# Kernel tuning notes

Measured on AMD Instinct MI355X. Metric: run time of the kernel, lower is better.

The kernel has to match this reference:

```python
import jax, jax.numpy as jnp
import numpy as np

B, T, C = 8, 2048, 1024
DFF = 4 * C
EPS = 1e-5


def _ln(h, w, b):
    mu = jnp.mean(h, axis=-1, keepdims=True)
    var = jnp.mean((h - mu) ** 2, axis=-1, keepdims=True)
    return (h - mu) * jax.lax.rsqrt(var + EPS) * w + b


def setup_inputs() -> dict:
    key = jax.random.key(0)
    ks = jax.random.split(key, 8)
    s = lambda fan_in: 1.0 / np.sqrt(fan_in)
    return {
        "x": jax.random.normal(ks[0], (B, T, C), jnp.float32),
        "w_router": jax.random.normal(ks[1], (1, C), jnp.float32) * s(C),
        "ln1_w": jnp.ones((C,), jnp.float32),
        "ln1_b": jnp.zeros((C,), jnp.float32),
        "w_qkv": jax.random.normal(ks[2], (3 * C, C), jnp.float32) * s(C),
        "b_qkv": jnp.zeros((3 * C,), jnp.float32),
        "w_o": jax.random.normal(ks[3], (C, C), jnp.float32) * s(C),
        "b_o": jnp.zeros((C,), jnp.float32),
        "ln2_w": jnp.ones((C,), jnp.float32),
        "ln2_b": jnp.zeros((C,), jnp.float32),
        "w_fc": jax.random.normal(ks[4], (DFF, C), jnp.float32) * s(C),
        "b_fc": jnp.zeros((DFF,), jnp.float32),
        "w_proj": jax.random.normal(ks[5], (C, DFF), jnp.float32) * s(DFF),
        "b_proj": jnp.zeros((C,), jnp.float32),
        "top_k": 1024,
        "n_head": 16,
    }


def _gpt2_block(h, ln1_w, ln1_b, w_qkv, b_qkv, w_o, b_o, ln2_w, ln2_b,
                w_fc, b_fc, w_proj, b_proj, n_head):
    Bq, S, Cm = h.shape
    dh = Cm // n_head
    a = _ln(h, ln1_w, ln1_b)
    qkv = a @ w_qkv.T + b_qkv                         # [B,S,3C]
    q, k, v = jnp.split(qkv, 3, axis=-1)
    q = q.reshape(Bq, S, n_head, dh)
    k = k.reshape(Bq, S, n_head, dh)
    v = v.reshape(Bq, S, n_head, dh)
    scores = jnp.einsum("bqhd,bkhd->bhqk", q, k) / np.sqrt(dh)
    causal = jnp.tril(jnp.ones((S, S), bool))
    scores = jnp.where(causal, scores, jnp.finfo(scores.dtype).min)
    probs = jax.nn.softmax(scores, axis=-1)
    attn = jnp.einsum("bhqk,bkhd->bqhd", probs, v).reshape(Bq, S, Cm)
    h = h + attn @ w_o.T + b_o
    m = _ln(h, ln2_w, ln2_b)
    mlp = jax.nn.gelu(m @ w_fc.T + b_fc, approximate=False) @ w_proj.T + b_proj
    return h + mlp


def reference(x, w_router, ln1_w, ln1_b, w_qkv, b_qkv, w_o, b_o,
              ln2_w, ln2_b, w_fc, b_fc, w_proj, b_proj, top_k, n_head):
    # STEP 1: router logits + top-k tokens (sorted by position)
    logits = (x @ w_router.T)[..., 0]                  # [B,T]
    weights, idx = jax.lax.top_k(logits, top_k)        # [B,K]
    order = jnp.argsort(idx, axis=1)
    idx = jnp.take_along_axis(idx, order, axis=1)
    weights = jnp.take_along_axis(weights, order, axis=1)
    # STEP 2: gather reduced sequence and run the block
    tokens = jnp.take_along_axis(x, idx[..., None], axis=1)   # [B,K,C]
    processed = _gpt2_block(tokens, ln1_w, ln1_b, w_qkv, b_qkv, w_o, b_o,
                            ln2_w, ln2_b, w_fc, b_fc, w_proj, b_proj, n_head)
    # STEP 3: weighted scatter-add combine
    src = processed * weights[..., None]
    out = jax.vmap(lambda xb, ib, sb: xb.at[ib].add(sb))(x, idx, src)
    return out
```

## Files before the change

kernel.cpp:

```cpp
#include <hip/hip_runtime.h>
#include <hip/hip_bf16.h>

#define B_ 8
#define T_ 2048
#define C_ 1024
#define S_ 1024
#define H_ 16
#define DH_ 64
#define DFF_ 4096
#define M_ (B_*S_)

typedef __attribute__((ext_vector_type(8))) short bf16x8;
typedef __attribute__((ext_vector_type(4))) float f32x4;

__device__ __forceinline__ short f2bf(float f) {
  __hip_bfloat16 h = __float2bfloat16(f);
  return *reinterpret_cast<short*>(&h);
}
__device__ __forceinline__ float bf2f(short s) {
  __hip_bfloat16 h = *reinterpret_cast<__hip_bfloat16*>(&s);
  return __bfloat162float(h);
}

typedef const __attribute__((address_space(1))) unsigned int* gas_p;
typedef __attribute__((address_space(3))) unsigned int* las_p;
__device__ __forceinline__ void gload_lds16(const void* g, void* l) {
  __builtin_amdgcn_global_load_lds((gas_p)g, (las_p)l, 16, 0, 0);
}

__global__ __launch_bounds__(256) void k_router(const float* __restrict__ x,
    const float* __restrict__ wr, float* __restrict__ logits) {
  int tok = blockIdx.x * 4 + (threadIdx.x >> 6);
  int l = threadIdx.x & 63;
  const float* xr = x + (size_t)tok * C_;
  float s = 0.f;
  #pragma unroll
  for (int j = 0; j < C_/64; ++j) s += xr[l + 64*j] * wr[l + 64*j];
  #pragma unroll
  for (int m = 32; m; m >>= 1) s += __shfl_xor(s, m);
  if (l == 0) logits[tok] = s;
}

__global__ __launch_bounds__(1024) void k_topk(const float* __restrict__ logits,
    int* __restrict__ idx, float* __restrict__ wts) {
  __shared__ unsigned long long key[2048];
  int b = blockIdx.x, t = threadIdx.x;
  for (int i = t; i < T_; i += 1024) {
    float v = logits[(size_t)b*T_ + i];
    unsigned u = __float_as_uint(v);
    unsigned so = u ^ ((u >> 31) ? 0xFFFFFFFFu : 0x80000000u);
    key[i] = ((unsigned long long)(~so) << 32) | (unsigned)i;
  }
  __syncthreads();
  for (int k = 2; k <= 2048; k <<= 1) {
    for (int j = k >> 1; j > 0; j >>= 1) {
      int i = ((t & ~(j-1)) << 1) | (t & (j-1));
      int ix = i | j;
      unsigned long long a = key[i], c = key[ix];
      bool up = ((i & k) == 0);
      if ((a > c) == up) { key[i] = c; key[ix] = a; }
      __syncthreads();
    }
  }
  unsigned long long a = key[t];
  __syncthreads();
  unsigned i0 = (unsigned)(a & 0xFFFFFFFFu);
  unsigned so = ~(unsigned)(a >> 32);
  unsigned bits = (so & 0x80000000u) ? (so ^ 0x80000000u) : ~so;
  key[t] = ((unsigned long long)i0 << 32) | bits;
  __syncthreads();
  for (int k = 2; k <= 1024; k <<= 1) {
    for (int j = k >> 1; j > 0; j >>= 1) {
      if (t < 512) {
        int i = ((t & ~(j-1)) << 1) | (t & (j-1));
        int ix = i | j;
        unsigned long long a2 = key[i], c2 = key[ix];
        bool up = ((i & k) == 0);
        if ((a2 > c2) == up) { key[i] = c2; key[ix] = a2; }
      }
      __syncthreads();
    }
  }
  idx[(size_t)b*S_ + t] = (int)(key[t] >> 32);
  wts[(size_t)b*S_ + t] = __uint_as_float((unsigned)(key[t] & 0xFFFFFFFFu));
}

__global__ __launch_bounds__(256) void k_cvt(const float* __restrict__ s,
    short* __restrict__ d, int n4) {
  int i = blockIdx.x * 256 + threadIdx.x;
  if (i >= n4) return;
  float4 v = ((const float4*)s)[i];
  short4 o;
  o.x = f2bf(v.x); o.y = f2bf(v.y); o.z = f2bf(v.z); o.w = f2bf(v.w);
  ((short4*)d)[i] = o;
}

template<bool GATHER>
__global__ __launch_bounds__(256) void k_ln(const float* __restrict__ x,
    const int* __restrict__ idx, float* __restrict__ hbuf,
    short* __restrict__ obf, const float* __restrict__ g,
    const float* __restrict__ beta) {
  __shared__ float red[8];
  int row = blockIdx.x;
  const float* src;
  if (GATHER) {
    int b = row >> 10, k = row & 1023;
    src = x + ((size_t)b*T_ + idx[b*S_ + k]) * C_;
  } else {
    src = hbuf + (size_t)row * C_;
  }
  int t = threadIdx.x;
  float4 v = *(const float4*)(src + t*4);
  float s  = v.x + v.y + v.z + v.w;
  float s2 = v.x*v.x + v.y*v.y + v.z*v.z + v.w*v.w;
  #pragma unroll
  for (int m = 32; m; m >>= 1) { s += __shfl_xor(s, m); s2 += __shfl_xor(s2, m); }
  int w = t >> 6, lane = t & 63;
  if (lane == 0) { red[w] = s; red[w+4] = s2; }
  __syncthreads();
  s  = red[0]+red[1]+red[2]+red[3];
  s2 = red[4]+red[5]+red[6]+red[7];
  float mu = s * (1.f/(float)C_);
  float var = s2 * (1.f/(float)C_) - mu*mu;
  float rs = rsqrtf(var + 1e-5f);
  int c0 = t*4;
  float4 gw = *(const float4*)(g + c0);
  float4 bw = *(const float4*)(beta + c0);
  short4 o;
  o.x = f2bf((v.x-mu)*rs*gw.x + bw.x);
  o.y = f2bf((v.y-mu)*rs*gw.y + bw.y);
  o.z = f2bf((v.z-mu)*rs*gw.z + bw.z);
  o.w = f2bf((v.w-mu)*rs*gw.w + bw.w);
  *(short4*)(obf + (size_t)row*C_ + c0) = o;
  if (GATHER) *(float4*)(hbuf + (size_t)row*C_ + c0) = v;
}

#define EPI_BF16 0
#define EPI_GELU 1
#define EPI_ADD32 2

__device__ __forceinline__ float gelu_fast(float v) {
  float z = 0.7978845608f * (v + 0.044715f * v * v * v);
  float e = __expf(2.f * z);
  return v - v * __builtin_amdgcn_rcpf(e + 1.f);
}

template<int BM, int BN, int EPI>
__global__ __launch_bounds__(256) void k_gemm4(
    const short* __restrict__ A, int lda,
    const short* __restrict__ Bp, int ldb,
    void* __restrict__ Cp, int ldc,
    const float* __restrict__ bias,
    int nNt, int Ktot) {
  constexpr int ACH = BM*64/8/256;
  constexpr int BCH = BN*64/8/256;
  __shared__ short As[BM*64];
  __shared__ short Bs[BN*64];
  int nwg = gridDim.x, orig = blockIdx.x;
  int q8 = nwg >> 3, r8 = nwg & 7;
  int xcd = orig & 7, loc = orig >> 3;
  int wg = (xcd < r8 ? xcd*(q8+1) : r8*(q8+1) + (xcd-r8)*q8) + loc;
  int bm = wg / nNt, bn = wg % nNt;
  const short* Ar = A + (size_t)bm*BM*lda;
  const short* Br = Bp + (size_t)bn*BN*ldb;
  constexpr int WM = BM/2, WN = BN/2, FM = WM/16, FN = WN/16;
  int t = threadIdx.x, lane = t & 63, w = t >> 6;
  int wm = w >> 1, wn = w & 1;
  int lr = lane & 15, kq = lane >> 4;
  f32x4 acc[FM][FN] = {};
  for (int k0 = 0; k0 < Ktot; k0 += 64) {
    #pragma unroll
    for (int c = 0; c < ACH; ++c) {
      int ch = c*256 + t;
      int row = ch >> 3, sq = (ch & 7) ^ (row & 7);
      gload_lds16(Ar + (size_t)row*lda + (k0 + sq*8), &As[ch*8]);
    }
    #pragma unroll
    for (int c = 0; c < BCH; ++c) {
      int ch = c*256 + t;
      int row = ch >> 3, sq = (ch & 7) ^ (row & 7);
      gload_lds16(Br + (size_t)row*ldb + (k0 + sq*8), &Bs[ch*8]);
    }
    asm volatile("s_waitcnt vmcnt(0)" ::: "memory");
    __syncthreads();
    bf16x8 af[2][FM], bfv[2][FN];
    #pragma unroll
    for (int ks = 0; ks < 2; ++ks) {
      #pragma unroll
      for (int i = 0; i < FM; ++i) {
        int ra = wm*WM + i*16 + lr;
        af[ks][i] = *(const bf16x8*)&As[ra*64 + ((((ks<<2)+kq) ^ (ra & 7)) << 3)];
      }
      #pragma unroll
      for (int j = 0; j < FN; ++j) {
        int rb = wn*WN + j*16 + lr;
        bfv[ks][j] = *(const bf16x8*)&Bs[rb*64 + ((((ks<<2)+kq) ^ (rb & 7)) << 3)];
      }
    }
    #pragma unroll
    for (int ks = 0; ks < 2; ++ks)
      #pragma unroll
      for (int i = 0; i < FM; ++i)
        #pragma unroll
        for (int j = 0; j < FN; ++j)
          acc[i][j] = __builtin_amdgcn_mfma_f32_16x16x32_bf16(bfv[ks][j], af[ks][i], acc[i][j], 0, 0, 0);
    __syncthreads();
  }
  int mrow0 = bm*BM + wm*WM + lr;
  int ncol0 = bn*BN + wn*WN + (kq << 2);
  #pragma unroll
  for (int i = 0; i < FM; ++i) {
    int row = mrow0 + i*16;
    #pragma unroll
    for (int j = 0; j < FN; ++j) {
      int col = ncol0 + j*16;
      float4 bv = bias ? *(const float4*)(bias + col) : make_float4(0.f,0.f,0.f,0.f);
      float v0 = acc[i][j][0] + bv.x, v1 = acc[i][j][1] + bv.y;
      float v2 = acc[i][j][2] + bv.z, v3 = acc[i][j][3] + bv.w;
      if (EPI == EPI_ADD32) {
        float* Co = (float*)Cp + (size_t)row*ldc + col;
        float4 old = *(float4*)Co;
        old.x += v0; old.y += v1; old.z += v2; old.w += v3;
        *(float4*)Co = old;
      } else {
        if (EPI == EPI_GELU) {
          v0 = gelu_fast(v0); v1 = gelu_fast(v1);
          v2 = gelu_fast(v2); v3 = gelu_fast(v3);
        }
        short4 o; o.x = f2bf(v0); o.y = f2bf(v1); o.z = f2bf(v2); o.w = f2bf(v3);
        *(short4*)((short*)Cp + (size_t)row*ldc + col) = o;
      }
    }
  }
}

__global__ __launch_bounds__(256) void k_vt(const short* __restrict__ qkv,
                                            short* __restrict__ vt) {
  __shared__ short tile[64][65];
  int blk = blockIdx.x;
  int s0 = (blk & 15) << 6;
  int bh = blk >> 4;
  int b = bh >> 4, h = bh & 15;
  const short* src = qkv + (size_t)b*S_*3*C_ + 2*C_ + h*DH_;
  int t = threadIdx.x;
  #pragma unroll
  for (int it = 0; it < 16; ++it) {
    int e = it*256 + t;
    int r = e >> 6, d = e & 63;
    tile[d][r] = src[(size_t)(s0 + r)*3*C_ + d];
  }
  __syncthreads();
  short* dst = vt + (size_t)bh*DH_*S_ + s0;
  #pragma unroll
  for (int it = 0; it < 16; ++it) {
    int e = it*256 + t;
    int d2 = e >> 6, c = e & 63;
    dst[(size_t)d2*S_ + c] = tile[d2][c];
  }
}

__global__ __launch_bounds__(256) void k_fattn(
    const short* __restrict__ qkv, const short* __restrict__ vt,
    short* __restrict__ attnb) {
  __shared__ short Ks[128*64];
  __shared__ short Vs[64*128];
  __shared__ short Ps[4][32*136];
  int qt = blockIdx.x;
  int bh = blockIdx.y;
  int b = bh >> 4, h = bh & 15;
  int t = threadIdx.x, lane = t & 63, w = t >> 6;
  int lr = lane & 15, kq = lane >> 4;
  const short* Qbase = qkv + ((size_t)b*S_ + qt*128)*3*C_ + h*DH_;
  const short* Kbase = qkv + (size_t)b*S_*3*C_ + C_ + h*DH_;
  const short* Vtb   = vt + (size_t)bh*DH_*S_;

  #pragma unroll
  for (int c = 0; c < 4; ++c) {
    int ch = c*256 + t;
    int row = ch >> 3, sq = (ch & 7) ^ (row & 7);
    gload_lds16(Qbase + (size_t)row*3*C_ + sq*8, &Ks[ch*8]);
  }
  asm volatile("s_waitcnt vmcnt(0)" ::: "memory");
  __syncthreads();
  bf16x8 qf[2][2];
  #pragma unroll
  for (int ks = 0; ks < 2; ++ks)
    #pragma unroll
    for (int i = 0; i < 2; ++i) {
      int rq = w*32 + i*16 + lr;
      qf[ks][i] = *(const bf16x8*)&Ks[rq*64 + ((((ks<<2)+kq) ^ (rq & 7)) << 3)];
    }
  __syncthreads();

  f32x4 o[2][4] = {};
  float m_i[2] = {-3.0e38f, -3.0e38f};
  float l_i[2] = {0.f, 0.f};
  short* Pw = &Ps[w][0];

  for (int j128 = 0; j128 <= qt; ++j128) {
    #pragma unroll
    for (int c = 0; c < 4; ++c) {
      int ch = c*256 + t;
      int row = ch >> 3, sq = (ch & 7) ^ (row & 7);
      gload_lds16(Kbase + (size_t)(j128*128 + row)*3*C_ + sq*8, &Ks[ch*8]);
    }
    #pragma unroll
    for (int c = 0; c < 4; ++c) {
      int ch = c*256 + t;
      int row = ch >> 4, cc = ch & 15, sq = cc ^ ((row & 7) << 1);
      gload_lds16(Vtb + (size_t)row*S_ + (j128*128 + sq*8), &Vs[ch*8]);
    }
    asm volatile("s_waitcnt vmcnt(0)" ::: "memory");
    __syncthreads();

    f32x4 s[2][8] = {};
    #pragma unroll
    for (int ks = 0; ks < 2; ++ks) {
      bf16x8 kf[8];
      #pragma unroll
      for (int j = 0; j < 8; ++j) {
        int rk = j*16 + lr;
        kf[j] = *(const bf16x8*)&Ks[rk*64 + ((((ks<<2)+kq) ^ (rk & 7)) << 3)];
      }
      #pragma unroll
      for (int i = 0; i < 2; ++i)
        #pragma unroll
        for (int j = 0; j < 8; ++j)
          s[i][j] = __builtin_amdgcn_mfma_f32_16x16x32_bf16(kf[j], qf[ks][i], s[i][j], 0, 0, 0);
    }

    bool diag = (j128 == qt);
    #pragma unroll
    for (int i = 0; i < 2; ++i) {
      int qrow = w*32 + i*16 + lr;
      float rmax = -3.0e38f;
      #pragma unroll
      for (int j = 0; j < 8; ++j)
        #pragma unroll
        for (int r = 0; r < 4; ++r) {
          int col = j*16 + (kq<<2) + r;
          float v = s[i][j][r] * 0.125f;
          if (diag && col > qrow) v = -3.0e38f;
          s[i][j][r] = v;
          rmax = fmaxf(rmax, v);
        }
      rmax = fmaxf(rmax, __shfl_xor(rmax, 16));
      rmax = fmaxf(rmax, __shfl_xor(rmax, 32));
      float mnew = fmaxf(m_i[i], rmax);
      float alpha = __expf(m_i[i] - mnew);
      m_i[i] = mnew;
      float rsum = 0.f;
      #pragma unroll
      for (int j = 0; j < 8; ++j)
        #pragma unroll
        for (int r = 0; r < 4; ++r) {
          float p = __expf(s[i][j][r] - mnew);
          s[i][j][r] = p;
          rsum += p;
        }
      rsum += __shfl_xor(rsum, 16);
      rsum += __shfl_xor(rsum, 32);
      l_i[i] = l_i[i]*alpha + rsum;
      #pragma unroll
      for (int jo = 0; jo < 4; ++jo)
        #pragma unroll
        for (int r = 0; r < 4; ++r)
          o[i][jo][r] *= alpha;
    }

    #pragma unroll
    for (int i = 0; i < 2; ++i)
      #pragma unroll
      for (int j = 0; j < 8; ++j) {
        short4 pk;
        pk.x = f2bf(s[i][j][0]); pk.y = f2bf(s[i][j][1]);
        pk.z = f2bf(s[i][j][2]); pk.w = f2bf(s[i][j][3]);
        int prow = i*16 + lr;
        *(short4*)&Pw[prow*136 + j*16 + (kq<<2)] = pk;
      }
    __syncthreads();

    #pragma unroll
    for (int sstep = 0; sstep < 4; ++sstep) {
      bf16x8 pf[2], vf[4];
      #pragma unroll
      for (int i = 0; i < 2; ++i) {
        int prow = i*16 + lr;
        pf[i] = *(const bf16x8*)&Pw[prow*136 + sstep*32 + (kq<<3)];
      }
      #pragma unroll
      for (int jo = 0; jo < 4; ++jo) {
        int rv = jo*16 + lr;
        int cc = (sstep*4 + kq) ^ ((rv & 7) << 1);
        vf[jo] = *(const bf16x8*)&Vs[rv*128 + cc*8];
      }
      #pragma unroll
      for (int i = 0; i < 2; ++i)
        #pragma unroll
        for (int jo = 0; jo < 4; ++jo)
          o[i][jo] = __builtin_amdgcn_mfma_f32_16x16x32_bf16(vf[jo], pf[i], o[i][jo], 0, 0, 0);
    }
    __syncthreads();
  }

  #pragma unroll
  for (int i = 0; i < 2; ++i) {
    float inv = 1.f / l_i[i];
    int q = qt*128 + w*32 + i*16 + lr;
    #pragma unroll
    for (int jo = 0; jo < 4; ++jo) {
      int d = jo*16 + (kq<<2);
      short4 ov;
      ov.x = f2bf(o[i][jo][0]*inv); ov.y = f2bf(o[i][jo][1]*inv);
      ov.z = f2bf(o[i][jo][2]*inv); ov.w = f2bf(o[i][jo][3]*inv);
      *(short4*)&attnb[((size_t)b*S_ + q)*C_ + h*DH_ + d] = ov;
    }
  }
}

__global__ void k_copy(const float* __restrict__ src, float* __restrict__ dst,
                       size_t n4) {
  size_t i = (size_t)blockIdx.x*256 + threadIdx.x;
  size_t stride = (size_t)gridDim.x*256;
  for (; i < n4; i += stride) ((float4*)dst)[i] = ((const float4*)src)[i];
}

__global__ __launch_bounds__(256) void k_scatter(const float* __restrict__ x,
    const int* __restrict__ idx, const float* __restrict__ wts,
    const float* __restrict__ hbuf, float* __restrict__ out) {
  int row = blockIdx.x;
  int b = row >> 10, k = row & 1023;
  int tk = idx[(size_t)b*S_ + k];
  float wv = wts[(size_t)b*S_ + k];
  size_t o  = ((size_t)b*T_ + tk)*C_ + threadIdx.x*4;
  size_t hs = (size_t)row*C_ + threadIdx.x*4;
  float4 xv = *(const float4*)(x + o);
  float4 hv = *(const float4*)(hbuf + hs);
  xv.x += wv*hv.x; xv.y += wv*hv.y; xv.z += wv*hv.z; xv.w += wv*hv.w;
  *(float4*)(out + o) = xv;
}

extern "C" void kernel_launch(void* const* d_in, const int* in_sizes, int n_in,
                              void* d_out, int out_size, void* d_ws, size_t ws_size,
                              hipStream_t stream) {
  const float* x     = (const float*)d_in[0];
  const float* wrt   = (const float*)d_in[1];
  const float* ln1w  = (const float*)d_in[2];
  const float* ln1b  = (const float*)d_in[3];
  const float* wqkv  = (const float*)d_in[4];
  const float* bqkv  = (const float*)d_in[5];
  const float* wo    = (const float*)d_in[6];
  const float* bo    = (const float*)d_in[7];
  const float* ln2w  = (const float*)d_in[8];
  const float* ln2b  = (const float*)d_in[9];
  const float* wfc   = (const float*)d_in[10];
  const float* bfc   = (const float*)d_in[11];
  const float* wproj = (const float*)d_in[12];
  const float* bproj = (const float*)d_in[13];
  float* out = (float*)d_out;

  char* p = (char*)d_ws;
  auto alloc = [&](size_t bytes) {
    char* r = p; p += (bytes + 255) & ~(size_t)255; return r;
  };
  float* logits = (float*)alloc((size_t)B_*T_*4);
  int*   idx    = (int*)  alloc((size_t)B_*S_*4);
  float* wts    = (float*)alloc((size_t)B_*S_*4);
  float* hbuf   = (float*)alloc((size_t)M_*C_*4);
  short* abuf   = (short*)alloc((size_t)M_*C_*2);
  short* qkvb   = (short*)alloc((size_t)M_*3*C_*2);
  short* vtb    = (short*)alloc((size_t)B_*H_*DH_*S_*2);
  short* attnb  = (short*)alloc((size_t)M_*C_*2);
  short* fcb    = (short*)alloc((size_t)M_*DFF_*2);
  short* wqkvb  = (short*)alloc((size_t)3*C_*C_*2);
  short* wob    = (short*)alloc((size_t)C_*C_*2);
  short* wfcb   = (short*)alloc((size_t)DFF_*C_*2);
  short* wprojb = (short*)alloc((size_t)C_*DFF_*2);
  if (ws_size < (size_t)(p - (char*)d_ws)) return;

  k_cvt<<<dim3(3*C_*C_/4/256), dim3(256), 0, stream>>>(wqkv, wqkvb, 3*C_*C_/4);
  k_cvt<<<dim3(C_*C_/4/256),   dim3(256), 0, stream>>>(wo, wob, C_*C_/4);
  k_cvt<<<dim3(DFF_*C_/4/256), dim3(256), 0, stream>>>(wfc, wfcb, DFF_*C_/4);
  k_cvt<<<dim3(C_*DFF_/4/256), dim3(256), 0, stream>>>(wproj, wprojb, C_*DFF_/4);

  k_router<<<dim3(B_*T_/4), dim3(256), 0, stream>>>(x, wrt, logits);
  k_topk<<<dim3(B_), dim3(1024), 0, stream>>>(logits, idx, wts);

  k_ln<true><<<dim3(M_), dim3(256), 0, stream>>>(x, idx, hbuf, abuf, ln1w, ln1b);

  k_gemm4<128,128,EPI_BF16>
    <<<dim3((M_/128)*(3*C_/128)), dim3(256), 0, stream>>>(
      abuf, C_, wqkvb, C_, qkvb, 3*C_, bqkv, 3*C_/128, C_);

  k_vt<<<dim3(B_*H_*(S_/64)), dim3(256), 0, stream>>>(qkvb, vtb);

  k_fattn<<<dim3(S_/128, B_*H_), dim3(256), 0, stream>>>(qkvb, vtb, attnb);

  k_gemm4<128,128,EPI_ADD32>
    <<<dim3((M_/128)*(C_/128)), dim3(256), 0, stream>>>(
      attnb, C_, wob, C_, hbuf, C_, bo, C_/128, C_);

  k_ln<false><<<dim3(M_), dim3(256), 0, stream>>>(nullptr, nullptr, hbuf, abuf, ln2w, ln2b);

  k_gemm4<128,128,EPI_GELU>
    <<<dim3((M_/128)*(DFF_/128)), dim3(256), 0, stream>>>(
      abuf, C_, wfcb, C_, fcb, DFF_, bfc, DFF_/128, C_);

  k_gemm4<128,128,EPI_ADD32>
    <<<dim3((M_/128)*(C_/128)), dim3(256), 0, stream>>>(
      fcb, DFF_, wprojb, DFF_, hbuf, C_, bproj, C_/128, DFF_);

  k_copy<<<dim3(2048), dim3(256), 0, stream>>>(x, out, (size_t)B_*T_*C_/4);
  k_scatter<<<dim3(M_), dim3(256), 0, stream>>>(x, idx, wts, hbuf, out);
}
```

Baseline: 560.5 us.

## Double-buffer 64-wide K tiles in flash attention, read V directly from global

```diff
diff --git a/kernel.cpp b/kernel.cpp
--- a/kernel.cpp
+++ b/kernel.cpp
@@ -259,12 +259,11 @@
   }
 }
 
-__global__ __launch_bounds__(256) void k_fattn(
+__global__ __launch_bounds__(256, 4) void k_fattn(
     const short* __restrict__ qkv, const short* __restrict__ vt,
     short* __restrict__ attnb) {
-  __shared__ short Ks[128*64];
-  __shared__ short Vs[64*128];
-  __shared__ short Ps[4][32*136];
+  __shared__ short Ks[2][64*64];
+  __shared__ short Ps[4][32*72];
   int qt = blockIdx.x;
   int bh = blockIdx.y;
   int b = bh >> 4, h = bh & 15;
@@ -274,73 +273,77 @@
   const short* Kbase = qkv + (size_t)b*S_*3*C_ + C_ + h*DH_;
   const short* Vtb   = vt + (size_t)bh*DH_*S_;
 
+  short* Qs = &Ks[0][0];
   #pragma unroll
   for (int c = 0; c < 4; ++c) {
     int ch = c*256 + t;
     int row = ch >> 3, sq = (ch & 7) ^ (row & 7);
-    gload_lds16(Qbase + (size_t)row*3*C_ + sq*8, &Ks[ch*8]);
+    gload_lds16(Qbase + (size_t)row*3*C_ + sq*8, &Qs[ch*8]);
   }
   asm volatile("s_waitcnt vmcnt(0)" ::: "memory");
-  __syncthreads();
+  __builtin_amdgcn_s_barrier();
   bf16x8 qf[2][2];
   #pragma unroll
   for (int ks = 0; ks < 2; ++ks)
     #pragma unroll
     for (int i = 0; i < 2; ++i) {
       int rq = w*32 + i*16 + lr;
-      qf[ks][i] = *(const bf16x8*)&Ks[rq*64 + ((((ks<<2)+kq) ^ (rq & 7)) << 3)];
-    }
-  __syncthreads();
+      qf[ks][i] = *(const bf16x8*)&Qs[rq*64 + ((((ks<<2)+kq) ^ (rq & 7)) << 3)];
+    }
+  asm volatile("s_waitcnt lgkmcnt(0)" ::: "memory");
+  __builtin_amdgcn_sched_barrier(0);
+  __builtin_amdgcn_s_barrier();
+
+  auto stageK = [&](int buf, int jj) {
+    #pragma unroll
+    for (int c = 0; c < 2; ++c) {
+      int ch = c*256 + t;
+      int row = ch >> 3, sq = (ch & 7) ^ (row & 7);
+      gload_lds16(Kbase + (size_t)(jj*64 + row)*3*C_ + sq*8, &Ks[buf][ch*8]);
+    }
+  };
+  stageK(0, 0);
 
   f32x4 o[2][4] = {};
   float m_i[2] = {-3.0e38f, -3.0e38f};
   float l_i[2] = {0.f, 0.f};
   short* Pw = &Ps[w][0];
-
-  for (int j128 = 0; j128 <= qt; ++j128) {
-    #pragma unroll
-    for (int c = 0; c < 4; ++c) {
-      int ch = c*256 + t;
-      int row = ch >> 3, sq = (ch & 7) ^ (row & 7);
-      gload_lds16(Kbase + (size_t)(j128*128 + row)*3*C_ + sq*8, &Ks[ch*8]);
-    }
-    #pragma unroll
-    for (int c = 0; c < 4; ++c) {
-      int ch = c*256 + t;
-      int row = ch >> 4, cc = ch & 15, sq = cc ^ ((row & 7) << 1);
-      gload_lds16(Vtb + (size_t)row*S_ + (j128*128 + sq*8), &Vs[ch*8]);
-    }
+  int NTl = 2*qt + 2;
+
+  for (int jj = 0; jj < NTl; ++jj) {
+    int cur = jj & 1;
     asm volatile("s_waitcnt vmcnt(0)" ::: "memory");
-    __syncthreads();
-
-    f32x4 s[2][8] = {};
+    __builtin_amdgcn_s_barrier();
+    if (jj + 1 < NTl) stageK(cur ^ 1, jj + 1);
+
+    f32x4 s[2][4] = {};
     #pragma unroll
     for (int ks = 0; ks < 2; ++ks) {
-      bf16x8 kf[8];
-      #pragma unroll
-      for (int j = 0; j < 8; ++j) {
+      bf16x8 kf[4];
+      #pragma unroll
+      for (int j = 0; j < 4; ++j) {
         int rk = j*16 + lr;
-        kf[j] = *(const bf16x8*)&Ks[rk*64 + ((((ks<<2)+kq) ^ (rk & 7)) << 3)];
+        kf[j] = *(const bf16x8*)&Ks[cur][rk*64 + ((((ks<<2)+kq) ^ (rk & 7)) << 3)];
       }
       #pragma unroll
       for (int i = 0; i < 2; ++i)
         #pragma unroll
-        for (int j = 0; j < 8; ++j)
+        for (int j = 0; j < 4; ++j)
           s[i][j] = __builtin_amdgcn_mfma_f32_16x16x32_bf16(kf[j], qf[ks][i], s[i][j], 0, 0, 0);
     }
 
-    bool diag = (j128 == qt);
+    bool maskTile = (jj >= 2*qt);
     #pragma unroll
     for (int i = 0; i < 2; ++i) {
-      int qrow = w*32 + i*16 + lr;
+      int qrow = qt*128 + w*32 + i*16 + lr;
       float rmax = -3.0e38f;
       #pragma unroll
-      for (int j = 0; j < 8; ++j)
+      for (int j = 0; j < 4; ++j)
         #pragma unroll
         for (int r = 0; r < 4; ++r) {
-          int col = j*16 + (kq<<2) + r;
+          int colg = jj*64 + j*16 + (kq<<2) + r;
           float v = s[i][j][r] * 0.125f;
-          if (diag && col > qrow) v = -3.0e38f;
+          if (maskTile && colg > qrow) v = -3.0e38f;
           s[i][j][r] = v;
           rmax = fmaxf(rmax, v);
         }
@@ -351,12 +354,12 @@
       m_i[i] = mnew;
       float rsum = 0.f;
       #pragma unroll
-      for (int j = 0; j < 8; ++j)
+      for (int j = 0; j < 4; ++j)
         #pragma unroll
         for (int r = 0; r < 4; ++r) {
-          float p = __expf(s[i][j][r] - mnew);
-          s[i][j][r] = p;
-          rsum += p;
+          float pv = __expf(s[i][j][r] - mnew);
+          s[i][j][r] = pv;
+          rsum += pv;
         }
       rsum += __shfl_xor(rsum, 16);
       rsum += __shfl_xor(rsum, 32);
@@ -371,36 +374,30 @@
     #pragma unroll
     for (int i = 0; i < 2; ++i)
       #pragma unroll
-      for (int j = 0; j < 8; ++j) {
+      for (int j = 0; j < 4; ++j) {
         short4 pk;
         pk.x = f2bf(s[i][j][0]); pk.y = f2bf(s[i][j][1]);
         pk.z = f2bf(s[i][j][2]); pk.w = f2bf(s[i][j][3]);
-        int prow = i*16 + lr;
-        *(short4*)&Pw[prow*136 + j*16 + (kq<<2)] = pk;
+        *(short4*)&Pw[(i*16 + lr)*72 + j*16 + (kq<<2)] = pk;
       }
-    __syncthreads();
-
-    #pragma unroll
-    for (int sstep = 0; sstep < 4; ++sstep) {
+    asm volatile("s_waitcnt lgkmcnt(0)" ::: "memory");
+    __builtin_amdgcn_sched_barrier(0);
+
+    #pragma unroll
+    for (int sstep = 0; sstep < 2; ++sstep) {
       bf16x8 pf[2], vf[4];
       #pragma unroll
-      for (int i = 0; i < 2; ++i) {
-        int prow = i*16 + lr;
-        pf[i] = *(const bf16x8*)&Pw[prow*136 + sstep*32 + (kq<<3)];
-      }
-      #pragma unroll
-      for (int jo = 0; jo < 4; ++jo) {
-        int rv = jo*16 + lr;
-        int cc = (sstep*4 + kq) ^ ((rv & 7) << 1);
-        vf[jo] = *(const bf16x8*)&Vs[rv*128 + cc*8];
-      }
+      for (int i = 0; i < 2; ++i)
+        pf[i] = *(const bf16x8*)&Pw[(i*16 + lr)*72 + sstep*32 + (kq<<3)];
+      #pragma unroll
+      for (int jo = 0; jo < 4; ++jo)
+        vf[jo] = *(const bf16x8*)&Vtb[(size_t)(jo*16 + lr)*S_ + jj*64 + sstep*32 + (kq<<3)];
       #pragma unroll
       for (int i = 0; i < 2; ++i)
         #pragma unroll
         for (int jo = 0; jo < 4; ++jo)
           o[i][jo] = __builtin_amdgcn_mfma_f32_16x16x32_bf16(vf[jo], pf[i], o[i][jo], 0, 0, 0);
     }
-    __syncthreads();
   }
 
   #pragma unroll
```

Result: faster. 533.5 us (-4.8%).
